# Kernel optimization log

Measured on AMD Instinct MI355X. Metric: run time of the kernel, lower is better.

The kernel has to match this reference:

```python
import jax, jax.numpy as jnp
import numpy as np

B, S, F = 64, 1024, 768          # batch, seq = num_patch*patch_size**2, d_model
H, DH = 12, 64                    # heads, head dim = out_dim // d
P2 = 64                           # patch_size ** 2 = attended window length
SCALE = 8.0                       # norm_scale ** 0.5 = (out_dim // d) ** 0.5


def setup_inputs() -> dict:
    key = jax.random.key(0)
    ks = jax.random.split(key, 10)
    std = 0.02
    return {
        "x": jax.random.normal(ks[0], (B, S, F), dtype=jnp.float32),
        # per-head q/k/v projection weights stacked: [H, DH, F] (Linear: y = x @ W.T + b)
        "Wq": jax.random.normal(ks[1], (H, DH, F), dtype=jnp.float32) * std,
        "bq": jax.random.normal(ks[2], (H, DH), dtype=jnp.float32) * std,
        "Wk": jax.random.normal(ks[3], (H, DH, F), dtype=jnp.float32) * std,
        "bk": jax.random.normal(ks[4], (H, DH), dtype=jnp.float32) * std,
        "Wv": jax.random.normal(ks[5], (H, DH, F), dtype=jnp.float32) * std,
        "bv": jax.random.normal(ks[6], (H, DH), dtype=jnp.float32) * std,
        # MHA output projection (only W_MSA[0] is ever used in the stage1 path)
        "Wo": jax.random.normal(ks[7], (F, F), dtype=jnp.float32) * std,
        "bo": jax.random.normal(ks[8], (F,), dtype=jnp.float32) * std,
    }


def reference(x, Wq, bq, Wk, bk, Wv, bv, Wo, bo):
    # stage1 path of SBlock1: only the first window (P2 tokens) goes through
    # MultiHeadAttention (W_MSA[0]); remaining windows are passed through raw
    # and concatenated along the sequence dim.
    xw = x[:, :P2, :]                                    # [B, P2, F]
    q = jnp.einsum('bsf,hdf->bhsd', xw, Wq) + bq[None, :, None, :]
    k = jnp.einsum('bsf,hdf->bhsd', xw, Wk) + bk[None, :, None, :]
    v = jnp.einsum('bsf,hdf->bhsd', xw, Wv) + bv[None, :, None, :]
    scores = jnp.einsum('bhsd,bhtd->bhst', q, k) / SCALE
    attn = jax.nn.softmax(scores, axis=-1)
    o = jnp.einsum('bhst,bhtd->bhsd', attn, v)           # [B, H, P2, DH]
    # heads concatenated along feature dim in order 0..H-1
    o = o.transpose(0, 2, 1, 3).reshape(xw.shape[0], P2, H * DH)
    o = o @ Wo.T + bo                                    # output projection
    return jnp.concatenate([o, x[:, P2:, :]], axis=1)    # [B, S, F]
```

## Files before the change

### kernel.cpp

```cpp
#include <hip/hip_runtime.h>

#define B_   64
#define S_   1024
#define F_   768
#define H_   12
#define DH_  64
#define P2_  64
#define NQKV 2304

using bf16x8 = __attribute__((ext_vector_type(8))) short;
using f32x4  = __attribute__((ext_vector_type(4))) float;

__device__ __forceinline__ unsigned short f2bf(float f) {
    union { float f; unsigned u; } v;
    v.f = f;
    unsigned r = v.u + 0x7FFF + ((v.u >> 16) & 1);
    return (unsigned short)(r >> 16);
}

__global__ __launch_bounds__(256) void copy_cast_kernel(
        const float* __restrict__ x, float* __restrict__ out,
        unsigned short* __restrict__ xw) {
    const int total4  = B_ * S_ * F_ / 4;
    const int batch4  = S_ * F_ / 4;
    const int window4 = P2_ * F_ / 4;
    int stride = gridDim.x * blockDim.x;
    for (int i = blockIdx.x * blockDim.x + threadIdx.x; i < total4; i += stride) {
        float4 v = reinterpret_cast<const float4*>(x)[i];
        int r = i % batch4;
        if (r >= window4) {
            reinterpret_cast<float4*>(out)[i] = v;
        } else {
            int b = i / batch4;
            ushort4 h;
            h.x = f2bf(v.x); h.y = f2bf(v.y); h.z = f2bf(v.z); h.w = f2bf(v.w);
            reinterpret_cast<ushort4*>(xw)[b * window4 + r] = h;
        }
    }
}

__global__ __launch_bounds__(256) void wcast_kernel(
        const float* __restrict__ Wq, const float* __restrict__ Wk,
        const float* __restrict__ Wv, const float* __restrict__ Wo,
        const float* __restrict__ bq, const float* __restrict__ bk,
        const float* __restrict__ bv,
        unsigned short* __restrict__ Wqkv, unsigned short* __restrict__ Wob,
        float* __restrict__ biasq) {
    const int W4     = 589824 / 4;
    const int total4 = 4 * W4 + 576;
    int stride = gridDim.x * blockDim.x;
    for (int i4 = blockIdx.x * blockDim.x + threadIdx.x; i4 < total4; i4 += stride) {
        if (i4 < 3 * W4) {
            int which = i4 / W4, local = i4 % W4;
            const float* src = (which == 0) ? Wq : (which == 1) ? Wk : Wv;
            float4 v = reinterpret_cast<const float4*>(src)[local];
            ushort4 h;
            h.x = f2bf(v.x); h.y = f2bf(v.y); h.z = f2bf(v.z); h.w = f2bf(v.w);
            reinterpret_cast<ushort4*>(Wqkv)[i4] = h;
        } else if (i4 < 4 * W4) {
            int local = i4 - 3 * W4;
            float4 v = reinterpret_cast<const float4*>(Wo)[local];
            ushort4 h;
            h.x = f2bf(v.x); h.y = f2bf(v.y); h.z = f2bf(v.z); h.w = f2bf(v.w);
            reinterpret_cast<ushort4*>(Wob)[local] = h;
        } else {
            int j4 = i4 - 4 * W4;
            int seg = j4 / 192, local = j4 % 192;
            const float* src = (seg == 0) ? bq : (seg == 1) ? bk : bv;
            reinterpret_cast<float4*>(biasq)[j4] =
                reinterpret_cast<const float4*>(src)[local];
        }
    }
}

template <int OUT_MODE>
__global__ __launch_bounds__(256) void gemm_kernel(
        const unsigned short* __restrict__ A, const unsigned short* __restrict__ Bw,
        const float* __restrict__ bias, void* __restrict__ Cout) {
    __shared__ __align__(16) unsigned char lds[32768];
    unsigned char* As = lds;
    unsigned char* Bs = lds + 16384;
    const int tid  = threadIdx.x;
    const int lane = tid & 63;
    const int w    = tid >> 6;
    const int wr   = w >> 1, wc = w & 1;
    const int m0 = blockIdx.y * 128, n0 = blockIdx.x * 128;
    const int ldc = gridDim.x << 7;

    f32x4 acc[4][4] = {};

    for (int kt = 0; kt < 768; kt += 64) {
        __syncthreads();
#pragma unroll
        for (int p = 0; p < 4; ++p) {
            int id  = p * 256 + tid;
            int row = id >> 3, c = id & 7;
            int4 va = *reinterpret_cast<const int4*>(A  + (m0 + row) * 768 + kt + c * 8);
            *reinterpret_cast<int4*>(As + row * 128 + ((c ^ (row & 7)) << 4)) = va;
            int4 vb = *reinterpret_cast<const int4*>(Bw + (n0 + row) * 768 + kt + c * 8);
            *reinterpret_cast<int4*>(Bs + row * 128 + ((c ^ (row & 7)) << 4)) = vb;
        }
        __syncthreads();
#pragma unroll
        for (int kk = 0; kk < 2; ++kk) {
            const int g = kk * 4 + (lane >> 4);
            bf16x8 a[4], b[4];
#pragma unroll
            for (int i = 0; i < 4; ++i) {
                int row = wr * 64 + i * 16 + (lane & 15);
                a[i] = *reinterpret_cast<const bf16x8*>(As + row * 128 + ((g ^ (row & 7)) << 4));
            }
#pragma unroll
            for (int j = 0; j < 4; ++j) {
                int row = wc * 64 + j * 16 + (lane & 15);
                b[j] = *reinterpret_cast<const bf16x8*>(Bs + row * 128 + ((g ^ (row & 7)) << 4));
            }
#pragma unroll
            for (int i = 0; i < 4; ++i)
#pragma unroll
                for (int j = 0; j < 4; ++j)
                    acc[i][j] = __builtin_amdgcn_mfma_f32_16x16x32_bf16(a[i], b[j], acc[i][j], 0, 0, 0);
        }
    }

    float bj[4];
#pragma unroll
    for (int j = 0; j < 4; ++j) bj[j] = bias[n0 + wc * 64 + j * 16 + (lane & 15)];

#pragma unroll
    for (int i = 0; i < 4; ++i) {
        int mrow = m0 + wr * 64 + i * 16 + ((lane >> 4) << 2);
#pragma unroll
        for (int j = 0; j < 4; ++j) {
            int n = n0 + wc * 64 + j * 16 + (lane & 15);
#pragma unroll
            for (int r = 0; r < 4; ++r) {
                float v = acc[i][j][r] + bj[j];
                if constexpr (OUT_MODE == 0) {
                    reinterpret_cast<unsigned short*>(Cout)[(mrow + r) * 2304 + n] = f2bf(v);
                } else {
                    int m = mrow + r;
                    reinterpret_cast<float*>(Cout)[(m >> 6) * 786432 + (m & 63) * 768 + n] = v;
                }
            }
        }
    }
}

__global__ __launch_bounds__(256) void attn_kernel(
        const unsigned short* __restrict__ Y, unsigned short* __restrict__ O) {
    const int bh = blockIdx.x;
    const int b = bh / 12, h = bh % 12;
    __shared__ __align__(16) unsigned char lds[32768];
    unsigned char* Qs = lds;
    unsigned char* Ks = lds + 8192;
    unsigned char* Vt = lds + 16384;
    unsigned char* Ps = lds + 24576;
    const int tid = threadIdx.x, lane = tid & 63, w = tid >> 6;

    for (int c = tid; c < 512; c += 256) {
        int row = c >> 3, cc = c & 7;
        const unsigned short* src = Y + (size_t)(b * 64 + row) * NQKV + h * 64 + cc * 8;
        *reinterpret_cast<int4*>(Qs + row * 128 + ((cc ^ (row & 7)) << 4)) =
            *reinterpret_cast<const int4*>(src);
        *reinterpret_cast<int4*>(Ks + row * 128 + ((cc ^ (row & 7)) << 4)) =
            *reinterpret_cast<const int4*>(src + 768);
        int4 vv = *reinterpret_cast<const int4*>(src + 1536);
        const unsigned short* vs = reinterpret_cast<const unsigned short*>(&vv);
#pragma unroll
        for (int u = 0; u < 8; ++u) {
            int d = cc * 8 + u;
            *reinterpret_cast<unsigned short*>(
                Vt + d * 128 + (((row >> 3) ^ u) << 4) + ((row & 7) << 1)) = vs[u];
        }
    }
    __syncthreads();

    f32x4 accS[4] = {};
#pragma unroll
    for (int kk = 0; kk < 2; ++kk) {
        const int g = kk * 4 + (lane >> 4);
        int qrow = w * 16 + (lane & 15);
        bf16x8 a = *reinterpret_cast<const bf16x8*>(Qs + qrow * 128 + ((g ^ (qrow & 7)) << 4));
#pragma unroll
        for (int j = 0; j < 4; ++j) {
            int krow = j * 16 + (lane & 15);
            bf16x8 bb = *reinterpret_cast<const bf16x8*>(Ks + krow * 128 + ((g ^ (krow & 7)) << 4));
            accS[j] = __builtin_amdgcn_mfma_f32_16x16x32_bf16(a, bb, accS[j], 0, 0, 0);
        }
    }

#pragma unroll
    for (int r = 0; r < 4; ++r) {
        float v0 = accS[0][r], v1 = accS[1][r], v2 = accS[2][r], v3 = accS[3][r];
        float mx = fmaxf(fmaxf(v0, v1), fmaxf(v2, v3));
        mx = fmaxf(mx, __shfl_xor(mx, 1));
        mx = fmaxf(mx, __shfl_xor(mx, 2));
        mx = fmaxf(mx, __shfl_xor(mx, 4));
        mx = fmaxf(mx, __shfl_xor(mx, 8));
        float p0 = __expf((v0 - mx) * 0.125f);
        float p1 = __expf((v1 - mx) * 0.125f);
        float p2 = __expf((v2 - mx) * 0.125f);
        float p3 = __expf((v3 - mx) * 0.125f);
        float sm = p0 + p1 + p2 + p3;
        sm += __shfl_xor(sm, 1);
        sm += __shfl_xor(sm, 2);
        sm += __shfl_xor(sm, 4);
        sm += __shfl_xor(sm, 8);
        float inv = 1.0f / sm;
        int srow = w * 16 + ((lane >> 4) << 2) + r;
        float pv[4] = {p0 * inv, p1 * inv, p2 * inv, p3 * inv};
#pragma unroll
        for (int j = 0; j < 4; ++j) {
            int t = j * 16 + (lane & 15);
            *reinterpret_cast<unsigned short*>(
                Ps + srow * 128 + (((t >> 3) ^ (srow & 7)) << 4) + ((t & 7) << 1)) = f2bf(pv[j]);
        }
    }
    __syncthreads();

    f32x4 accO[4] = {};
#pragma unroll
    for (int kk = 0; kk < 2; ++kk) {
        const int g = kk * 4 + (lane >> 4);
        int prow = w * 16 + (lane & 15);
        bf16x8 a = *reinterpret_cast<const bf16x8*>(Ps + prow * 128 + ((g ^ (prow & 7)) << 4));
#pragma unroll
        for (int j = 0; j < 4; ++j) {
            int drow = j * 16 + (lane & 15);
            bf16x8 bb = *reinterpret_cast<const bf16x8*>(Vt + drow * 128 + ((g ^ (drow & 7)) << 4));
            accO[j] = __builtin_amdgcn_mfma_f32_16x16x32_bf16(a, bb, accO[j], 0, 0, 0);
        }
    }

#pragma unroll
    for (int j = 0; j < 4; ++j) {
        int d = h * 64 + j * 16 + (lane & 15);
#pragma unroll
        for (int r = 0; r < 4; ++r) {
            int s = w * 16 + ((lane >> 4) << 2) + r;
            O[(size_t)(b * 64 + s) * 768 + d] = f2bf(accO[j][r]);
        }
    }
}

extern "C" void kernel_launch(void* const* d_in, const int* in_sizes, int n_in,
                              void* d_out, int out_size, void* d_ws, size_t ws_size,
                              hipStream_t stream) {
    const float* x  = (const float*)d_in[0];
    const float* Wq = (const float*)d_in[1];
    const float* bq = (const float*)d_in[2];
    const float* Wk = (const float*)d_in[3];
    const float* bk = (const float*)d_in[4];
    const float* Wv = (const float*)d_in[5];
    const float* bv = (const float*)d_in[6];
    const float* Wo = (const float*)d_in[7];
    const float* bo = (const float*)d_in[8];
    float* out = (float*)d_out;
    char* ws = (char*)d_ws;

    unsigned short* xw   = (unsigned short*)(ws);
    unsigned short* Wqkv = (unsigned short*)(ws + 6291456);
    unsigned short* Wob  = (unsigned short*)(ws + 9830400);
    float*          bqv  = (float*)(ws + 11010048);
    unsigned short* Y    = (unsigned short*)(ws + 11019264);
    unsigned short* Obuf = (unsigned short*)(ws + 29893632);

    copy_cast_kernel<<<2048, 256, 0, stream>>>(x, out, xw);
    wcast_kernel<<<1024, 256, 0, stream>>>(Wq, Wk, Wv, Wo, bq, bk, bv, Wqkv, Wob, bqv);
    gemm_kernel<0><<<dim3(18, 32), 256, 0, stream>>>(xw, Wqkv, bqv, (void*)Y);
    attn_kernel<<<768, 256, 0, stream>>>(Y, Obuf);
    gemm_kernel<1><<<dim3(6, 32), 256, 0, stream>>>(Obuf, Wob, bo, (void*)out);
}
```

Baseline: 414.5 us.

## Overlap passthrough copy with QKV GEMM and use direct global-to-LDS loads

```diff
diff --git a/kernel.cpp b/kernel.cpp
--- a/kernel.cpp
+++ b/kernel.cpp
@@ -18,133 +18,160 @@
     return (unsigned short)(r >> 16);
 }
 
-__global__ __launch_bounds__(256) void copy_cast_kernel(
-        const float* __restrict__ x, float* __restrict__ out,
-        unsigned short* __restrict__ xw) {
-    const int total4  = B_ * S_ * F_ / 4;
-    const int batch4  = S_ * F_ / 4;
-    const int window4 = P2_ * F_ / 4;
-    int stride = gridDim.x * blockDim.x;
-    for (int i = blockIdx.x * blockDim.x + threadIdx.x; i < total4; i += stride) {
-        float4 v = reinterpret_cast<const float4*>(x)[i];
-        int r = i % batch4;
-        if (r >= window4) {
-            reinterpret_cast<float4*>(out)[i] = v;
-        } else {
-            int b = i / batch4;
-            ushort4 h;
-            h.x = f2bf(v.x); h.y = f2bf(v.y); h.z = f2bf(v.z); h.w = f2bf(v.w);
-            reinterpret_cast<ushort4*>(xw)[b * window4 + r] = h;
-        }
-    }
-}
-
-__global__ __launch_bounds__(256) void wcast_kernel(
+__device__ __forceinline__ void gll16(const unsigned short* g, unsigned char* l) {
+    __builtin_amdgcn_global_load_lds(
+        (const __attribute__((address_space(1))) unsigned int*)g,
+        (__attribute__((address_space(3))) unsigned int*)l, 16, 0, 0);
+}
+
+__global__ __launch_bounds__(256) void prep_kernel(
+        const float* __restrict__ x,
         const float* __restrict__ Wq, const float* __restrict__ Wk,
         const float* __restrict__ Wv, const float* __restrict__ Wo,
         const float* __restrict__ bq, const float* __restrict__ bk,
         const float* __restrict__ bv,
-        unsigned short* __restrict__ Wqkv, unsigned short* __restrict__ Wob,
-        float* __restrict__ biasq) {
-    const int W4     = 589824 / 4;
-    const int total4 = 4 * W4 + 576;
-    int stride = gridDim.x * blockDim.x;
-    for (int i4 = blockIdx.x * blockDim.x + threadIdx.x; i4 < total4; i4 += stride) {
-        if (i4 < 3 * W4) {
-            int which = i4 / W4, local = i4 % W4;
-            const float* src = (which == 0) ? Wq : (which == 1) ? Wk : Wv;
-            float4 v = reinterpret_cast<const float4*>(src)[local];
-            ushort4 h;
-            h.x = f2bf(v.x); h.y = f2bf(v.y); h.z = f2bf(v.z); h.w = f2bf(v.w);
-            reinterpret_cast<ushort4*>(Wqkv)[i4] = h;
-        } else if (i4 < 4 * W4) {
-            int local = i4 - 3 * W4;
-            float4 v = reinterpret_cast<const float4*>(Wo)[local];
-            ushort4 h;
-            h.x = f2bf(v.x); h.y = f2bf(v.y); h.z = f2bf(v.z); h.w = f2bf(v.w);
-            reinterpret_cast<ushort4*>(Wob)[local] = h;
-        } else {
-            int j4 = i4 - 4 * W4;
-            int seg = j4 / 192, local = j4 % 192;
-            const float* src = (seg == 0) ? bq : (seg == 1) ? bk : bv;
-            reinterpret_cast<float4*>(biasq)[j4] =
-                reinterpret_cast<const float4*>(src)[local];
-        }
-    }
-}
-
-template <int OUT_MODE>
-__global__ __launch_bounds__(256) void gemm_kernel(
+        unsigned short* __restrict__ xw, unsigned short* __restrict__ Wqkv,
+        unsigned short* __restrict__ Wob, float* __restrict__ bqv) {
+    const int NW = 786432;
+    const int W4 = 147456;
+    int i = blockIdx.x * 256 + threadIdx.x;
+    if (i < NW) {
+        int b = i / 12288, r = i - b * 12288;
+        float4 v = reinterpret_cast<const float4*>(x)[b * 196608 + r];
+        ushort4 h;
+        h.x = f2bf(v.x); h.y = f2bf(v.y); h.z = f2bf(v.z); h.w = f2bf(v.w);
+        reinterpret_cast<ushort4*>(xw)[i] = h;
+    } else if (i < NW + 3 * W4) {
+        int j = i - NW;
+        int which = j / W4, local = j - which * W4;
+        const float* src = (which == 0) ? Wq : (which == 1) ? Wk : Wv;
+        float4 v = reinterpret_cast<const float4*>(src)[local];
+        ushort4 h;
+        h.x = f2bf(v.x); h.y = f2bf(v.y); h.z = f2bf(v.z); h.w = f2bf(v.w);
+        reinterpret_cast<ushort4*>(Wqkv)[j] = h;
+    } else if (i < NW + 4 * W4) {
+        int local = i - NW - 3 * W4;
+        float4 v = reinterpret_cast<const float4*>(Wo)[local];
+        ushort4 h;
+        h.x = f2bf(v.x); h.y = f2bf(v.y); h.z = f2bf(v.z); h.w = f2bf(v.w);
+        reinterpret_cast<ushort4*>(Wob)[local] = h;
+    } else if (i < NW + 4 * W4 + 576) {
+        int j4 = i - NW - 4 * W4;
+        int seg = j4 / 192, local = j4 - seg * 192;
+        const float* src = (seg == 0) ? bq : (seg == 1) ? bk : bv;
+        reinterpret_cast<float4*>(bqv)[j4] =
+            reinterpret_cast<const float4*>(src)[local];
+    }
+}
+
+template <int BM, int BN, int OUT_MODE>
+__device__ __forceinline__ void gemm_body(
+        int bx, int by,
         const unsigned short* __restrict__ A, const unsigned short* __restrict__ Bw,
         const float* __restrict__ bias, void* __restrict__ Cout) {
-    __shared__ __align__(16) unsigned char lds[32768];
+    constexpr int WC = (BN == 128) ? 2 : 1;
+    constexpr int WR = 4 / WC;
+    constexpr int MI = BM / WR / 16;
+    constexpr int NJ = BN / WC / 16;
+    constexpr int CA = BM / 32;
+    constexpr int CB = BN / 32;
+    __shared__ __align__(16) unsigned char lds[(BM + BN) * 128];
     unsigned char* As = lds;
-    unsigned char* Bs = lds + 16384;
+    unsigned char* Bs = lds + BM * 128;
     const int tid  = threadIdx.x;
     const int lane = tid & 63;
     const int w    = tid >> 6;
-    const int wr   = w >> 1, wc = w & 1;
-    const int m0 = blockIdx.y * 128, n0 = blockIdx.x * 128;
-    const int ldc = gridDim.x << 7;
-
-    f32x4 acc[4][4] = {};
+    const int wr = w / WC, wc = w % WC;
+    const int mbase = wr * (BM / WR), nbase = wc * (BN / WC);
+    const int m0 = by * BM, n0 = bx * BN;
+    const int lr = lane >> 3, lc = lane & 7;
+
+    f32x4 acc[MI][NJ] = {};
 
     for (int kt = 0; kt < 768; kt += 64) {
         __syncthreads();
 #pragma unroll
-        for (int p = 0; p < 4; ++p) {
-            int id  = p * 256 + tid;
-            int row = id >> 3, c = id & 7;
-            int4 va = *reinterpret_cast<const int4*>(A  + (m0 + row) * 768 + kt + c * 8);
-            *reinterpret_cast<int4*>(As + row * 128 + ((c ^ (row & 7)) << 4)) = va;
-            int4 vb = *reinterpret_cast<const int4*>(Bw + (n0 + row) * 768 + kt + c * 8);
-            *reinterpret_cast<int4*>(Bs + row * 128 + ((c ^ (row & 7)) << 4)) = vb;
+        for (int p = 0; p < CA; ++p) {
+            int row = (w * CA + p) * 8 + lr;
+            gll16(A + (size_t)(m0 + row) * 768 + kt + ((lc ^ (row & 7)) << 3),
+                  As + (w * CA + p) * 1024);
+        }
+#pragma unroll
+        for (int p = 0; p < CB; ++p) {
+            int row = (w * CB + p) * 8 + lr;
+            gll16(Bw + (size_t)(n0 + row) * 768 + kt + ((lc ^ (row & 7)) << 3),
+                  Bs + (w * CB + p) * 1024);
         }
         __syncthreads();
 #pragma unroll
         for (int kk = 0; kk < 2; ++kk) {
             const int g = kk * 4 + (lane >> 4);
-            bf16x8 a[4], b[4];
-#pragma unroll
-            for (int i = 0; i < 4; ++i) {
-                int row = wr * 64 + i * 16 + (lane & 15);
+            bf16x8 a[MI], b[NJ];
+#pragma unroll
+            for (int i = 0; i < MI; ++i) {
+                int row = mbase + i * 16 + (lane & 15);
                 a[i] = *reinterpret_cast<const bf16x8*>(As + row * 128 + ((g ^ (row & 7)) << 4));
             }
 #pragma unroll
-            for (int j = 0; j < 4; ++j) {
-                int row = wc * 64 + j * 16 + (lane & 15);
+            for (int j = 0; j < NJ; ++j) {
+                int row = nbase + j * 16 + (lane & 15);
                 b[j] = *reinterpret_cast<const bf16x8*>(Bs + row * 128 + ((g ^ (row & 7)) << 4));
             }
 #pragma unroll
-            for (int i = 0; i < 4; ++i)
-#pragma unroll
-                for (int j = 0; j < 4; ++j)
+            for (int i = 0; i < MI; ++i)
+#pragma unroll
+                for (int j = 0; j < NJ; ++j)
                     acc[i][j] = __builtin_amdgcn_mfma_f32_16x16x32_bf16(a[i], b[j], acc[i][j], 0, 0, 0);
         }
     }
 
-    float bj[4];
-#pragma unroll
-    for (int j = 0; j < 4; ++j) bj[j] = bias[n0 + wc * 64 + j * 16 + (lane & 15)];
-
-#pragma unroll
-    for (int i = 0; i < 4; ++i) {
-        int mrow = m0 + wr * 64 + i * 16 + ((lane >> 4) << 2);
-#pragma unroll
-        for (int j = 0; j < 4; ++j) {
-            int n = n0 + wc * 64 + j * 16 + (lane & 15);
+    float bj[NJ];
+#pragma unroll
+    for (int j = 0; j < NJ; ++j) bj[j] = bias[n0 + nbase + j * 16 + (lane & 15)];
+
+#pragma unroll
+    for (int i = 0; i < MI; ++i) {
+        int mrow = m0 + mbase + i * 16 + ((lane >> 4) << 2);
+#pragma unroll
+        for (int j = 0; j < NJ; ++j) {
+            int n = n0 + nbase + j * 16 + (lane & 15);
 #pragma unroll
             for (int r = 0; r < 4; ++r) {
                 float v = acc[i][j][r] + bj[j];
                 if constexpr (OUT_MODE == 0) {
-                    reinterpret_cast<unsigned short*>(Cout)[(mrow + r) * 2304 + n] = f2bf(v);
+                    reinterpret_cast<unsigned short*>(Cout)[(size_t)(mrow + r) * 2304 + n] = f2bf(v);
                 } else {
                     int m = mrow + r;
-                    reinterpret_cast<float*>(Cout)[(m >> 6) * 786432 + (m & 63) * 768 + n] = v;
+                    reinterpret_cast<float*>(Cout)[(size_t)(m >> 6) * 786432 + (m & 63) * 768 + n] = v;
                 }
             }
         }
     }
+}
+
+__global__ __launch_bounds__(256) void mega_kernel(
+        const float* __restrict__ x, float* __restrict__ out,
+        const unsigned short* __restrict__ xw, const unsigned short* __restrict__ Wqkv,
+        const float* __restrict__ bqv, unsigned short* __restrict__ Y) {
+    if (blockIdx.x < 2048) {
+        const int total4 = 11796480;
+        int stride = 2048 * 256;
+        for (int i = blockIdx.x * 256 + threadIdx.x; i < total4; i += stride) {
+            int b = i / 184320, r = i - b * 184320;
+            int idx = b * 196608 + 12288 + r;
+            reinterpret_cast<float4*>(out)[idx] =
+                reinterpret_cast<const float4*>(x)[idx];
+        }
+    } else {
+        int gid = blockIdx.x - 2048;
+        gemm_body<128, 128, 0>(gid % 18, gid / 18, xw, Wqkv, bqv, (void*)Y);
+    }
+}
+
+__global__ __launch_bounds__(256) void oproj_kernel(
+        const unsigned short* __restrict__ Obuf, const unsigned short* __restrict__ Wob,
+        const float* __restrict__ bo, float* __restrict__ out) {
+    gemm_body<64, 64, 1>(blockIdx.x, blockIdx.y, Obuf, Wob, bo, (void*)out);
 }
 
 __global__ __launch_bounds__(256) void attn_kernel(
@@ -266,9 +293,9 @@
     unsigned short* Y    = (unsigned short*)(ws + 11019264);
     unsigned short* Obuf = (unsigned short*)(ws + 29893632);
 
-    copy_cast_kernel<<<2048, 256, 0, stream>>>(x, out, xw);
-    wcast_kernel<<<1024, 256, 0, stream>>>(Wq, Wk, Wv, Wo, bq, bk, bv, Wqkv, Wob, bqv);
-    gemm_kernel<0><<<dim3(18, 32), 256, 0, stream>>>(xw, Wqkv, bqv, (void*)Y);
+    prep_kernel<<<5379, 256, 0, stream>>>(x, Wq, Wk, Wv, Wo, bq, bk, bv,
+                                          xw, Wqkv, Wob, bqv);
+    mega_kernel<<<2624, 256, 0, stream>>>(x, out, xw, Wqkv, bqv, Y);
     attn_kernel<<<768, 256, 0, stream>>>(Y, Obuf);
-    gemm_kernel<1><<<dim3(6, 32), 256, 0, stream>>>(Obuf, Wob, bo, (void*)out);
-}
+    oproj_kernel<<<dim3(12, 64), 256, 0, stream>>>(Obuf, Wob, bo, out);
+}
```

After: 414.0 us. Within noise of the previous version (-0.1%).
